# Kernel tuning notes

Hardware: AMD Instinct MI355X
Metric: run time of the kernel (lower is better)

The kernel has to match this reference:

```python
import jax, jax.numpy as jnp
import numpy as np

# static module hyperparameters (match init_kwargs)
DIMS = 1024
HEAD = 16
HD = DIMS // HEAD          # 64
MAX_ITER = 3
MIN_SIZE = 64
MAX_SIZE = 2048
UP_WIN, DOWN_WIN = 1.1, 0.9
UP_DIFF, DOWN_DIFF = 0.05, 0.001
B, T = 2, 1024


def _ln(x, w, eps=1e-5):
    # torch LayerNorm with bias=False (weight only), biased variance
    m = jnp.mean(x, axis=-1, keepdims=True)
    v = jnp.var(x, axis=-1, keepdims=True)
    return (x - m) * jax.lax.rsqrt(v + eps) * w


def setup_inputs() -> dict:
    key = jax.random.key(0)
    ks = jax.random.split(key, 12)

    def lin_w(k, o, i):
        return (jax.random.normal(k, (o, i), dtype=jnp.float32) / np.sqrt(i)).astype(jnp.float32)

    return {
        "x": jax.random.normal(ks[0], (B, T, DIMS), dtype=jnp.float32),
        "Wq": lin_w(ks[1], DIMS, DIMS), "bq": jnp.zeros((DIMS,), jnp.float32),
        "Wk": lin_w(ks[2], DIMS, DIMS),
        "Wv": lin_w(ks[3], DIMS, DIMS), "bv": jnp.zeros((DIMS,), jnp.float32),
        "Wo": lin_w(ks[4], DIMS, DIMS), "bo": jnp.zeros((DIMS,), jnp.float32),
        "lna_w": jnp.ones((DIMS,), jnp.float32),
        "lnb_w": jnp.ones((DIMS,), jnp.float32),
        "lnc_w": jnp.ones((HD,), jnp.float32),
        "lnd_w": jnp.ones((HD,), jnp.float32),
        "lq_w": lin_w(ks[5], HD, HD), "lq_b": jnp.zeros((HD,), jnp.float32),
        "lk_w": lin_w(ks[6], HD, HD), "lk_b": jnp.zeros((HD,), jnp.float32),
        "lv_w": lin_w(ks[7], HD, HD), "lv_b": jnp.zeros((HD,), jnp.float32),
        "threshold": jnp.float32(0.01),
        "temp_base": jnp.float32(1.0),
        "factor": jnp.float32(0.1),
    }


def _focus(x, Wq, bq, Wk, Wv, bv, Wo, bo, lna_w, lnb_w, lnc_w, lnd_w,
           lq_w, lq_b, lk_w, lk_b, lv_w, lv_b, threshold, temp_base, factor):
    b, t, d = x.shape
    q = _ln(x, lna_w) @ Wq.T + bq
    kk = _ln(x, lnb_w) @ Wk.T
    v = _ln(x, lnb_w) @ Wv.T + bv
    sc = HD ** (-0.25)

    def _shape(u):
        return u.reshape(b, t, HEAD, HD).transpose(0, 2, 1, 3)  # [B,H,T,hd]

    q_full = _shape(q * sc)
    k_full = _shape(kk * sc)
    v_full = _shape(v)

    # .item() calls in torch detach these from the graph
    thr = jax.lax.stop_gradient(threshold)
    fac = jax.lax.stop_gradient(factor)
    t0 = jax.lax.stop_gradient(temp_base)

    cw0 = jnp.int32(max(min(t, MAX_SIZE), MIN_SIZE))
    inv_sqrt_e = jnp.float32(1.0 / np.sqrt(HD))  # SDPA default scale
    pos = jnp.arange(t)

    def step(carry, i):
        qcur, prev, attn, cw, temp, done = carry
        # LocalOut projections over full length (out-of-window part masked below)
        qp = qcur @ lq_w.T + lq_b
        kp = k_full @ lk_w.T + lk_b
        vp = v_full @ lv_w.T + lv_b
        sq = _ln(qp, lnc_w)
        sk = _ln(kp, lnd_w)
        tscale = jnp.where(temp > 0, jax.lax.rsqrt(temp), jnp.float32(1.0))
        sq = sq * tscale
        scores = jnp.einsum('bhqd,bhkd->bhqk', sq, sk) * inv_sqrt_e
        in_win = pos < cw
        scores = jnp.where(in_win[None, None, None, :], scores, -jnp.inf)
        probs = jax.nn.softmax(scores, axis=-1)
        out = jnp.einsum('bhqk,bhkd->bhqd', probs, vp)
        # rows >= cur_win stay zero (iter_out buffer semantics)
        iter_out = jnp.where(in_win[None, None, :, None], out, 0.0)

        diff = jnp.mean(jnp.abs(iter_out - prev))
        converged = (diff < thr + fac * diff) & (i > 0)
        upd = (~done) & (~converged)            # continue iterating
        new_done = done | converged

        attn_n = jnp.where(done, attn, iter_out)
        prev_n = jnp.where(upd, iter_out, prev)
        qcur_n = jnp.where(upd, qcur + iter_out, qcur)
        # _next_win
        up = (cw.astype(jnp.float32) * UP_WIN).astype(jnp.int32)
        down = (cw.astype(jnp.float32) * DOWN_WIN).astype(jnp.int32)
        nw = jnp.where(diff > UP_DIFF, up,
                       jnp.where((diff < DOWN_DIFF) & (cw > MIN_SIZE), down, cw))
        nw = jnp.clip(nw, MIN_SIZE, t)
        cw_n = jnp.where(upd, nw, cw)
        temp_n = jnp.where(upd, temp + jnp.float32(0.005), temp)
        return (qcur_n, prev_n, attn_n, cw_n, temp_n, new_done), None

    zeros = jnp.zeros_like(q_full)
    carry0 = (q_full, zeros, zeros, cw0, t0, jnp.array(False))
    (_, _, attn_out, _, _, _), _ = jax.lax.scan(step, carry0, jnp.arange(MAX_ITER))

    output = attn_out.transpose(0, 2, 1, 3).reshape(b, t, d)
    return output @ Wo.T + bo


def reference(x, Wq, bq, Wk, Wv, bv, Wo, bo, lna_w, lnb_w, lnc_w, lnd_w,
              lq_w, lq_b, lk_w, lk_b, lv_w, lv_b, threshold, temp_base, factor):
    return _focus(x, Wq, bq, Wk, Wv, bv, Wo, bo, lna_w, lnb_w, lnc_w, lnd_w,
                  lq_w, lq_b, lk_w, lk_b, lv_w, lv_b, threshold, temp_base, factor)
```

## Files before the change

kernel.cpp:

```cpp
#include <hip/hip_runtime.h>
#include <hip/hip_bf16.h>

#define BDIM 2
#define TDIM 1024
#define DDIM 1024
#define HDIM 16
#define HD   64
#define RROWS (BDIM * TDIM)
#define BH    (BDIM * HDIM)
#define NHE   (BH * TDIM * HD)
#define NHE4  (NHE / 4)
#define DIFF_BLOCKS 512
#define L2E 1.4426950408889634f

typedef __attribute__((ext_vector_type(8))) short short8v;
typedef __attribute__((ext_vector_type(4))) short short4v;
typedef __attribute__((ext_vector_type(8))) _Float16 half8v;
typedef __attribute__((ext_vector_type(4))) _Float16 half4v;
typedef __attribute__((ext_vector_type(4))) float f32x4;

struct FState {
  int   cw;
  float temp;
  int   done;
  int   upd;
  int   done_prev;
  float thr;
  float fac;
  int   pad;
};

static __device__ __forceinline__ unsigned short f2bf(float x) {
  __hip_bfloat16 h = __float2bfloat16(x);
  return __builtin_bit_cast(unsigned short, h);
}
static __device__ __forceinline__ void gload16(const void* g, void* l) {
  __builtin_amdgcn_global_load_lds(
      (const __attribute__((address_space(1))) void*)g,
      (__attribute__((address_space(3))) void*)l, 16, 0, 0);
}

__global__ void init_kernel(FState* st, const float* thr, const float* tb, const float* fac) {
  if (threadIdx.x == 0 && blockIdx.x == 0) {
    st->cw = TDIM;
    st->temp = tb[0];
    st->done = 0;
    st->done_prev = 0;
    st->upd = 1;
    st->thr = thr[0];
    st->fac = fac[0];
  }
}

__global__ __launch_bounds__(256) void ln_x_kernel(
    const float* __restrict__ x, const float* __restrict__ wa, const float* __restrict__ wb,
    _Float16* __restrict__ xaH, _Float16* __restrict__ xbH)
{
  const int row = blockIdx.x;
  const int tid = threadIdx.x;
  const float4 v = reinterpret_cast<const float4*>(x + (size_t)row * DDIM)[tid];
  float s = v.x + v.y + v.z + v.w;
  float q = v.x * v.x + v.y * v.y + v.z * v.z + v.w * v.w;
#pragma unroll
  for (int off = 1; off < 64; off <<= 1) {
    s += __shfl_xor(s, off);
    q += __shfl_xor(q, off);
  }
  __shared__ float ss[4], qq[4];
  const int lane = tid & 63, wv = tid >> 6;
  if (lane == 0) { ss[wv] = s; qq[wv] = q; }
  __syncthreads();
  s = ss[0] + ss[1] + ss[2] + ss[3];
  q = qq[0] + qq[1] + qq[2] + qq[3];
  const float mean = s * (1.0f / DDIM);
  const float var  = q * (1.0f / DDIM) - mean * mean;
  const float inv  = rsqrtf(var + 1e-5f);
  const float4 a4 = reinterpret_cast<const float4*>(wa)[tid];
  const float4 b4 = reinterpret_cast<const float4*>(wb)[tid];
  const float hv[4] = { (v.x - mean) * inv, (v.y - mean) * inv,
                        (v.z - mean) * inv, (v.w - mean) * inv };
  const float av[4] = { a4.x, a4.y, a4.z, a4.w };
  const float bv[4] = { b4.x, b4.y, b4.z, b4.w };
  half4v ha, hb;
#pragma unroll
  for (int j = 0; j < 4; ++j) {
    ha[j] = (_Float16)(hv[j] * av[j]);
    hb[j] = (_Float16)(hv[j] * bv[j]);
  }
  *reinterpret_cast<half4v*>(xaH + (size_t)row * DDIM + tid * 4) = ha;
  *reinterpret_cast<half4v*>(xbH + (size_t)row * DDIM + tid * 4) = hb;
}

__global__ __launch_bounds__(256) void w_cvt_kernel(
    const float* __restrict__ W0, const float* __restrict__ W1,
    const float* __restrict__ W2, const float* __restrict__ W3,
    const float* __restrict__ W4,
    _Float16* __restrict__ O0, _Float16* __restrict__ O1,
    _Float16* __restrict__ O2, _Float16* __restrict__ O3,
    _Float16* __restrict__ O4)
{
  const float* W; _Float16* O;
  switch (blockIdx.y) {
    case 0:  W = W0; O = O0; break;
    case 1:  W = W1; O = O1; break;
    case 2:  W = W2; O = O2; break;
    case 3:  W = W3; O = O3; break;
    default:
      if (blockIdx.x >= 4) return;
      W = W4; O = O4; break;
  }
  const int r = blockIdx.x;
  const int tid = threadIdx.x;
  const float4 v = reinterpret_cast<const float4*>(W + (size_t)r * 1024)[tid];
  half4v h;
  h[0] = (_Float16)v.x; h[1] = (_Float16)v.y;
  h[2] = (_Float16)v.z; h[3] = (_Float16)v.w;
  *reinterpret_cast<half4v*>(O + (size_t)r * 1024 + tid * 4) = h;
}

template<int CMODE>
__global__ __launch_bounds__(256) void gemm_mfma_kernel(
    const _Float16* __restrict__ A0, const _Float16* __restrict__ W0,
    const float* __restrict__ b0, float* __restrict__ C0, float s0,
    const _Float16* __restrict__ A1, const _Float16* __restrict__ W1,
    const float* __restrict__ b1, float* __restrict__ C1, float s1,
    const _Float16* __restrict__ A2, const _Float16* __restrict__ W2,
    const float* __restrict__ b2, float* __restrict__ C2, float s2)
{
  const _Float16* A; const _Float16* W; const float* bias; float* C; float scale;
  switch (blockIdx.z) {
    case 0:  A = A0; W = W0; bias = b0; C = C0; scale = s0; break;
    case 1:  A = A1; W = W1; bias = b1; C = C1; scale = s1; break;
    default: A = A2; W = W2; bias = b2; C = C2; scale = s2; break;
  }
  __shared__ __align__(16) _Float16 As[128 * 32];
  __shared__ __align__(16) _Float16 Ws[128 * 32];
  const int tid = threadIdx.x;
  const int wv = tid >> 6, lane = tid & 63;
  const int wm = wv >> 1, wn = wv & 1;
  const int bm = blockIdx.x;
  const int bn = blockIdx.y;

  const _Float16* gA[2]; const _Float16* gW[2];
  _Float16* lA[2]; _Float16* lW[2];
#pragma unroll
  for (int j = 0; j < 2; ++j) {
    const int chunk = wv * 2 + j;
    const int r = chunk * 16 + (lane >> 2);
    const int ce = (lane & 3) * 8;
    gA[j] = A + (size_t)(bm * 128 + r) * 1024 + ce;
    gW[j] = W + (size_t)(bn * 128 + r) * 1024 + ce;
    lA[j] = As + chunk * 512;
    lW[j] = Ws + chunk * 512;
  }

  f32x4 acc[4][4] = {};
  const int rb = lane & 15;
  const int kb = (lane >> 4) * 8;

  for (int ks = 0; ks < 1024; ks += 32) {
    __syncthreads();
#pragma unroll
    for (int j = 0; j < 2; ++j) {
      gload16(gA[j] + ks, lA[j]);
      gload16(gW[j] + ks, lW[j]);
    }
    __syncthreads();
    half8v af[4], wf[4];
#pragma unroll
    for (int f = 0; f < 4; ++f) {
      af[f] = *reinterpret_cast<const half8v*>(As + (wm * 64 + f * 16 + rb) * 32 + kb);
      wf[f] = *reinterpret_cast<const half8v*>(Ws + (wn * 64 + f * 16 + rb) * 32 + kb);
    }
#pragma unroll
    for (int i = 0; i < 4; ++i)
#pragma unroll
      for (int j2 = 0; j2 < 4; ++j2)
        acc[i][j2] = __builtin_amdgcn_mfma_f32_16x16x32_f16(af[i], wf[j2], acc[i][j2], 0, 0, 0);
  }

#pragma unroll
  for (int j2 = 0; j2 < 4; ++j2) {
    const int n = bn * 128 + wn * 64 + j2 * 16 + (lane & 15);
    const float bv_ = bias ? bias[n] : 0.0f;
#pragma unroll
    for (int i = 0; i < 4; ++i) {
#pragma unroll
      for (int r = 0; r < 4; ++r) {
        const int m = bm * 128 + wm * 64 + i * 16 + (lane >> 4) * 4 + r;
        const float v = (acc[i][j2][r] + bv_) * scale;
        size_t ci;
        if constexpr (CMODE == 0) {
          ci = (size_t)m * 1024 + n;
        } else {
          const int b = m >> 10, t = m & (TDIM - 1);
          ci = ((size_t)(b * HDIM + (n >> 6)) * TDIM + t) * HD + (n & 63);
        }
        C[ci] = v;
      }
    }
  }
}

template<int OUT_MODE, bool DO_LN>
static __device__ __forceinline__ void headproj_body(
    const float* __restrict__ in, unsigned short* __restrict__ out,
    const float* __restrict__ w, const float* __restrict__ bias,
    const float* __restrict__ lnw, float* wl, unsigned short* tT)
{
  const int tid = threadIdx.x;
  for (int idx = tid; idx < 4096; idx += 256) {
    const int d = idx >> 6, i = idx & 63;
    wl[i * 65 + d] = w[idx];
  }
  const int lane = tid & 63, wv = tid >> 6;
  const float bd = bias[lane];
  float lw = 1.0f;
  if constexpr (DO_LN) lw = lnw[lane];
  __syncthreads();
  const int rowBase = blockIdx.x * 32 + wv * 8;
  for (int rr = 0; rr < 8; ++rr) {
    const int row = rowBase + rr;
    const float h = in[(size_t)row * HD + lane];
    float y = bd;
#pragma unroll
    for (int i = 0; i < 64; ++i) {
      const float hv = __uint_as_float((unsigned)__builtin_amdgcn_readlane((int)__float_as_uint(h), i));
      y += wl[i * 65 + lane] * hv;
    }
    if constexpr (DO_LN) {
      float s = y;
#pragma unroll
      for (int off = 1; off < 64; off <<= 1) s += __shfl_xor(s, off);
      const float mean = s * (1.0f / 64.0f);
      const float t0 = y - mean;
      float v2 = t0 * t0;
#pragma unroll
      for (int off = 1; off < 64; off <<= 1) v2 += __shfl_xor(v2, off);
      y = t0 * rsqrtf(v2 * (1.0f / 64.0f) + 1e-5f) * lw;
    }
    if constexpr (OUT_MODE == 0) {
      out[(size_t)row * HD + lane] = f2bf(y);
    } else {
      tT[lane * 34 + wv * 8 + rr] = f2bf(y);
    }
  }
  if constexpr (OUT_MODE == 1) {
    __syncthreads();
    const int hd = tid >> 2, tseg = (tid & 3) * 8;
    const int r0 = blockIdx.x * 32;
    const int bh = r0 >> 10, t0 = r0 & (TDIM - 1);
    short8v v;
#pragma unroll
    for (int i = 0; i < 8; ++i) v[i] = (short)tT[hd * 34 + tseg + i];
    *reinterpret_cast<short8v*>(out + ((size_t)bh * HD + hd) * TDIM + t0 + tseg) = v;
  }
}

__global__ __launch_bounds__(256) void headproj_kv_kernel(
    const float* __restrict__ kin, unsigned short* __restrict__ skb,
    const float* __restrict__ lkw, const float* __restrict__ lkb,
    const float* __restrict__ lnd,
    const float* __restrict__ vin, unsigned short* __restrict__ vpT,
    const float* __restrict__ lvw, const float* __restrict__ lvb)
{
  __shared__ float wl[64 * 65];
  __shared__ unsigned short tT[64 * 34];
  if (blockIdx.y == 0)
    headproj_body<0, true >(kin, skb, lkw, lkb, lnd, wl, tT);
  else
    headproj_body<1, false>(vin, vpT, lvw, lvb, (const float*)nullptr, wl, tT);
}

__global__ __launch_bounds__(512) void attn_mfma_kernel(
    const float* __restrict__ qcur, const unsigned short* __restrict__ sk,
    const unsigned short* __restrict__ vpT, float* __restrict__ io,
    const float* __restrict__ prev, _Float16* __restrict__ attnH,
    const _Float16* __restrict__ lqwH, const float* __restrict__ lqb,
    const float* __restrict__ lnc, float* __restrict__ partials,
    const FState* __restrict__ st, int is_first)
{
  if (st->done) return;
  const int lid = blockIdx.x;
  const int xcd = lid & 7;
  const int rr_ = lid >> 3;
  const int qb  = rr_ & 15;
  const int bh  = (rr_ >> 4) * 8 + xcd;

  const int cw = st->cw;
  const int tid = threadIdx.x;
  const int wv = tid >> 6, lane = tid & 63;
  const int wq = wv & 3, wk = wv >> 2;
  const int ql = lane & 15, hi = lane >> 4;
  const int qbase = qb * 64 + wq * 16;
  const int q = qbase + ql;
  const size_t baseRow = (size_t)bh * TDIM * HD;
  const size_t baseT   = (size_t)bh * HD * TDIM;
  float* orow = io + baseRow + (size_t)q * HD;
  const float* prow = prev + baseRow + (size_t)q * HD;
  float* qcrow = const_cast<float*>(qcur) + baseRow + (size_t)q * HD;
  const bool wvalid = (qbase < cw);
  _Float16* arow = attnH + (size_t)((bh >> 4) * TDIM + q) * 1024 + (bh & 15) * HD;

  __shared__ __align__(16) unsigned char KV[2][2][2][8192];
  __shared__ __align__(16) unsigned char PJ[8][2048];
  float* wred = reinterpret_cast<float*>(&KV[1][1][0][0]);

  const int sub  = lane >> 3;
  const int colB = (lane & 7) * 16;
  const int scol = (colB ^ (sub << 4)) >> 1;

  const int kb0 = wk * 512;
  const unsigned short* kSrc0 = sk  + baseRow + (size_t)(kb0 + wq * 16 + sub) * HD + scol;
  const unsigned short* vSrc0 = vpT + baseT  + (size_t)(wq * 16 + sub) * TDIM + scol;

  unsigned char* pj = (unsigned char*)PJ[wv];
  const unsigned swz8 = (unsigned)((ql & 7) << 4);

  const int nch0 = (min(cw, 512) + 63) >> 6;
  const int nch1 = (cw > 512) ? ((cw - 512 + 63) >> 6) : 0;
  const int nchOwn = wk ? nch1 : nch0;

  if (nchOwn > 0) {
#pragma unroll
    for (int jj = 0; jj < 2; ++jj) {
      gload16(kSrc0 + (size_t)(jj * 8) * HD, &KV[wk][0][0][(wq * 2 + jj) * 1024]);
      gload16(vSrc0 + (size_t)(jj * 8) * TDIM + kb0, &KV[wk][0][1][(wq * 2 + jj) * 1024]);
    }
  }

  short8v qf0, qf1;
  if (wvalid) {
    const float tp = st->temp;
    const float ts = (tp > 0.0f ? rsqrtf(tp) : 1.0f) * 0.125f;
    half8v qh0, qh1;
    {
      const f32x4 a0 = *reinterpret_cast<const f32x4*>(qcrow + hi * 8);
      const f32x4 a1 = *reinterpret_cast<const f32x4*>(qcrow + hi * 8 + 4);
      const f32x4 b0 = *reinterpret_cast<const f32x4*>(qcrow + 32 + hi * 8);
      const f32x4 b1 = *reinterpret_cast<const f32x4*>(qcrow + 32 + hi * 8 + 4);
#pragma unroll
      for (int j = 0; j < 4; ++j) {
        qh0[j] = (_Float16)a0[j]; qh0[4 + j] = (_Float16)a1[j];
        qh1[j] = (_Float16)b0[j]; qh1[4 + j] = (_Float16)b1[j];
      }
    }
    f32x4 sp[4];
#pragma unroll
    for (int f = 0; f < 4; ++f) {
      const half8v a0 = *reinterpret_cast<const half8v*>(lqwH + (f * 16 + ql) * 64 + hi * 8);
      const half8v a1 = *reinterpret_cast<const half8v*>(lqwH + (f * 16 + ql) * 64 + 32 + hi * 8);
      f32x4 acc = {};
      acc = __builtin_amdgcn_mfma_f32_16x16x32_f16(a0, qh0, acc, 0, 0, 0);
      acc = __builtin_amdgcn_mfma_f32_16x16x32_f16(a1, qh1, acc, 0, 0, 0);
      sp[f] = acc;
    }
    float sum = 0.f;
#pragma unroll
    for (int f = 0; f < 4; ++f) {
      const f32x4 b4 = *reinterpret_cast<const f32x4*>(lqb + f * 16 + hi * 4);
      sp[f] += b4;
      sum += (sp[f][0] + sp[f][1]) + (sp[f][2] + sp[f][3]);
    }
    sum += __shfl_xor(sum, 16);
    sum += __shfl_xor(sum, 32);
    const float mean = sum * (1.0f / 64.0f);
    float vs = 0.f;
#pragma unroll
    for (int f = 0; f < 4; ++f) {
#pragma unroll
      for (int r = 0; r < 4; ++r) {
        const float t0 = sp[f][r] - mean;
        sp[f][r] = t0;
        vs += t0 * t0;
      }
    }
    vs += __shfl_xor(vs, 16);
    vs += __shfl_xor(vs, 32);
    const float inv = rsqrtf(vs * (1.0f / 64.0f) + 1e-5f);
    const unsigned wb = (unsigned)(ql * 128 + hi * 8);
#pragma unroll
    for (int f = 0; f < 4; ++f) {
      const f32x4 lc = *reinterpret_cast<const f32x4*>(lnc + f * 16 + hi * 4);
      const float y0 = sp[f][0] * inv * lc[0] * ts;
      const float y1 = sp[f][1] * inv * lc[1] * ts;
      const float y2 = sp[f][2] * inv * lc[2] * ts;
      const float y3 = sp[f][3] * inv * lc[3] * ts;
      *reinterpret_cast<unsigned*>(pj + ((wb + f * 32)     ^ swz8)) =
          (unsigned)f2bf(y0) | ((unsigned)f2bf(y1) << 16);
      *reinterpret_cast<unsigned*>(pj + ((wb + f * 32 + 4) ^ swz8)) =
          (unsigned)f2bf(y2) | ((unsigned)f2bf(y3) << 16);
    }
    qf0 = *reinterpret_cast<short8v*>(pj + ((unsigned)(ql * 128 + hi * 16) ^ swz8));
    qf1 = *reinterpret_cast<short8v*>(pj + ((unsigned)(ql * 128 + 64 + hi * 16) ^ swz8));
  }
  __syncthreads();

  float m = -1e30f, l = 0.f;
  f32x4 o[4] = {};
  int cur = 0;
  for (int ch = 0; ch < nch0; ++ch) {
    if (ch + 1 < nchOwn) {
      const size_t kn = (size_t)(ch + 1) * 64;
#pragma unroll
      for (int jj = 0; jj < 2; ++jj) {
        gload16(kSrc0 + (kn + (size_t)(jj * 8)) * HD, &KV[wk][cur ^ 1][0][(wq * 2 + jj) * 1024]);
        gload16(vSrc0 + (size_t)(jj * 8) * TDIM + kb0 + kn, &KV[wk][cur ^ 1][1][(wq * 2 + jj) * 1024]);
      }
    }
    if (wvalid && ch < nchOwn) {
      const int k0 = kb0 + ch * 64;
      const unsigned char* kt = &KV[wk][cur][0][0];
      const unsigned char* vt = &KV[wk][cur][1][0];
      f32x4 s[4];
#pragma unroll
      for (int f = 0; f < 4; ++f) {
        const unsigned rb = (unsigned)((f * 16 + ql) * 128);
        const short8v a0 = *reinterpret_cast<const short8v*>(kt + rb + ((unsigned)(hi * 16) ^ swz8));
        const short8v a1 = *reinterpret_cast<const short8v*>(kt + rb + ((unsigned)(64 + hi * 16) ^ swz8));
        f32x4 acc = {};
        acc = __builtin_amdgcn_mfma_f32_16x16x32_bf16(a0, qf0, acc, 0, 0, 0);
        acc = __builtin_amdgcn_mfma_f32_16x16x32_bf16(a1, qf1, acc, 0, 0, 0);
        s[f] = acc;
      }
      float mc = -1e30f;
      if (k0 + 64 > cw) {
#pragma unroll
        for (int f = 0; f < 4; ++f)
#pragma unroll
          for (int r = 0; r < 4; ++r) {
            float v = s[f][r];
            if (k0 + f * 16 + hi * 4 + r >= cw) v = -1e30f;
            s[f][r] = v;
            mc = fmaxf(mc, v);
          }
      } else {
#pragma unroll
        for (int f = 0; f < 4; ++f)
#pragma unroll
          for (int r = 0; r < 4; ++r) mc = fmaxf(mc, s[f][r]);
      }
      mc = fmaxf(mc, __shfl_xor(mc, 16));
      mc = fmaxf(mc, __shfl_xor(mc, 32));
      if (__any(mc > m + 8.0f)) {
        const float mn = fmaxf(m, mc);
        const float c = __builtin_amdgcn_exp2f((m - mn) * L2E);
        l *= c;
#pragma unroll
        for (int f = 0; f < 4; ++f) o[f] *= c;
        m = mn;
      }
      float ls = 0.f;
      unsigned pk[8];
#pragma unroll
      for (int f = 0; f < 4; ++f) {
        const float p0 = __builtin_amdgcn_exp2f((s[f][0] - m) * L2E);
        const float p1 = __builtin_amdgcn_exp2f((s[f][1] - m) * L2E);
        const float p2 = __builtin_amdgcn_exp2f((s[f][2] - m) * L2E);
        const float p3 = __builtin_amdgcn_exp2f((s[f][3] - m) * L2E);
        ls += (p0 + p1) + (p2 + p3);
        pk[f * 2]     = (unsigned)f2bf(p0) | ((unsigned)f2bf(p1) << 16);
        pk[f * 2 + 1] = (unsigned)f2bf(p2) | ((unsigned)f2bf(p3) << 16);
      }
      ls += __shfl_xor(ls, 16);
      ls += __shfl_xor(ls, 32);
      l += ls;
      const unsigned wb = (unsigned)(ql * 128 + hi * 8);
#pragma unroll
      for (int f = 0; f < 4; ++f) {
        *reinterpret_cast<unsigned*>(pj + ((wb + f * 32)     ^ swz8)) = pk[f * 2];
        *reinterpret_cast<unsigned*>(pj + ((wb + f * 32 + 4) ^ swz8)) = pk[f * 2 + 1];
      }
#pragma unroll
      for (int kh = 0; kh < 2; ++kh) {
        const short8v pb = *reinterpret_cast<short8v*>(
            pj + ((unsigned)(ql * 128 + kh * 64 + hi * 16) ^ swz8));
#pragma unroll
        for (int f = 0; f < 4; ++f) {
          const unsigned rb = (unsigned)((f * 16 + ql) * 128);
          const short8v av = *reinterpret_cast<const short8v*>(
              vt + rb + ((unsigned)(kh * 64 + hi * 16) ^ swz8));
          o[f] = __builtin_amdgcn_mfma_f32_16x16x32_bf16(av, pb, o[f], 0, 0, 0);
        }
      }
    }
    __syncthreads();
    cur ^= 1;
  }

  float* Obuf = reinterpret_cast<float*>(&KV[0][0][0][0]);
  if (wk == 1 && wvalid) {
    if (hi == 0) {
      Obuf[4352 + wq * 16 + ql] = m;
      Obuf[4416 + wq * 16 + ql] = l;
    }
#pragma unroll
    for (int f = 0; f < 4; ++f)
      *reinterpret_cast<f32x4*>(&Obuf[(wq * 16 + ql) * 68 + f * 16 + hi * 4]) = o[f];
  }
  __syncthreads();

  float pd = 0.0f;
  if (wk == 0) {
    if (wvalid) {
      const float m1 = Obuf[4352 + wq * 16 + ql];
      const float l1 = Obuf[4416 + wq * 16 + ql];
      const float mn = fmaxf(m, m1);
      const float c0 = __builtin_amdgcn_exp2f((m - mn) * L2E);
      const float c1 = __builtin_amdgcn_exp2f((m1 - mn) * L2E);
      const float lt = l * c0 + l1 * c1;
      const bool valid = (q < cw);
      const float invl = valid ? (1.0f / lt) : 0.0f;
#pragma unroll
      for (int f = 0; f < 4; ++f) {
        const f32x4 o1 = *reinterpret_cast<const f32x4*>(&Obuf[(wq * 16 + ql) * 68 + f * 16 + hi * 4]);
        const f32x4 vo = (o[f] * c0 + o1 * c1) * invl;
        *reinterpret_cast<f32x4*>(orow + f * 16 + hi * 4) = vo;
        half4v h4;
        h4[0] = (_Float16)vo[0]; h4[1] = (_Float16)vo[1];
        h4[2] = (_Float16)vo[2]; h4[3] = (_Float16)vo[3];
        *reinterpret_cast<half4v*>(arow + f * 16 + hi * 4) = h4;
        const f32x4 qv = *reinterpret_cast<const f32x4*>(qcrow + f * 16 + hi * 4);
        *reinterpret_cast<f32x4*>(qcrow + f * 16 + hi * 4) = qv + vo;
        if (!is_first) {
          const f32x4 pv = *reinterpret_cast<const f32x4*>(prow + f * 16 + hi * 4);
          pd += fabsf(vo[0] - pv[0]) + fabsf(vo[1] - pv[1]) +
                fabsf(vo[2] - pv[2]) + fabsf(vo[3] - pv[3]);
        } else {
          pd += fabsf(vo[0]) + fabsf(vo[1]) + fabsf(vo[2]) + fabsf(vo[3]);
        }
      }
    } else {
      const f32x4 z = {0.f, 0.f, 0.f, 0.f};
      const half4v hz = { (_Float16)0.f, (_Float16)0.f, (_Float16)0.f, (_Float16)0.f };
#pragma unroll
      for (int f = 0; f < 4; ++f) {
        *reinterpret_cast<f32x4*>(orow + f * 16 + hi * 4) = z;
        *reinterpret_cast<half4v*>(arow + f * 16 + hi * 4) = hz;
        if (!is_first) {
          const f32x4 pv = *reinterpret_cast<const f32x4*>(prow + f * 16 + hi * 4);
          pd += fabsf(pv[0]) + fabsf(pv[1]) + fabsf(pv[2]) + fabsf(pv[3]);
        }
      }
    }
  }

#pragma unroll
  for (int off = 1; off < 64; off <<= 1) pd += __shfl_xor(pd, off);
  if (lane == 0) wred[wv] = pd;
  __syncthreads();
  if (tid == 0)
    partials[lid] = wred[0] + wred[1] + wred[2] + wred[3] +
                    wred[4] + wred[5] + wred[6] + wred[7];
}

__global__ __launch_bounds__(256) void state_update_kernel(
    FState* __restrict__ st, const float* __restrict__ partials, int iter)
{
  const int tid = threadIdx.x;
  float s = 0.0f;
  for (int i = tid; i < DIFF_BLOCKS; i += 256) s += partials[i];
  __shared__ float red[256];
  red[tid] = s;
  __syncthreads();
  for (int off = 128; off > 0; off >>= 1) {
    if (tid < off) red[tid] += red[tid + off];
    __syncthreads();
  }
  if (tid == 0) {
    const int done_prev = st->done;
    st->done_prev = done_prev;
    if (!done_prev) {
      const float diff = red[0] * (1.0f / (float)NHE);
      const bool conv = (diff < st->thr + st->fac * diff) && (iter > 0);
      st->upd  = conv ? 0 : 1;
      st->done = conv ? 1 : 0;
      if (!conv) {
        const int cw = st->cw;
        const int up = (int)((float)cw * 1.1f);
        const int dn = (int)((float)cw * 0.9f);
        int nw = (diff > 0.05f) ? up : ((diff < 0.001f && cw > 64) ? dn : cw);
        nw = nw < 64 ? 64 : (nw > TDIM ? TDIM : nw);
        st->cw = nw;
        st->temp += 0.005f;
      }
    } else {
      st->upd = 0;
    }
  }
}

extern "C" void kernel_launch(void* const* d_in, const int* in_sizes, int n_in,
                              void* d_out, int out_size, void* d_ws, size_t ws_size,
                              hipStream_t stream)
{
  const float* x   = (const float*)d_in[0];
  const float* Wq  = (const float*)d_in[1];
  const float* bq  = (const float*)d_in[2];
  const float* Wk  = (const float*)d_in[3];
  const float* Wv  = (const float*)d_in[4];
  const float* bv  = (const float*)d_in[5];
  const float* Wo  = (const float*)d_in[6];
  const float* bo  = (const float*)d_in[7];
  const float* lna = (const float*)d_in[8];
  const float* lnb = (const float*)d_in[9];
  const float* lnc = (const float*)d_in[10];
  const float* lnd = (const float*)d_in[11];
  const float* lqw = (const float*)d_in[12];
  const float* lqb = (const float*)d_in[13];
  const float* lkw = (const float*)d_in[14];
  const float* lkb = (const float*)d_in[15];
  const float* lvw = (const float*)d_in[16];
  const float* lvb = (const float*)d_in[17];
  const float* thr = (const float*)d_in[18];
  const float* tb  = (const float*)d_in[19];
  const float* fac = (const float*)d_in[20];
  float* out = (float*)d_out;

  float* f0   = (float*)d_ws;
  float* qcur = f0;
  float* io0  = f0 + (size_t)NHE;
  float* io1  = f0 + 2 * (size_t)NHE;
  _Float16* h0   = (_Float16*)(f0 + 3 * (size_t)NHE);
  _Float16* xaH  = h0;
  _Float16* attnH = h0;
  _Float16* xbH  = h0 + (size_t)RROWS * 1024;
  _Float16* WqH  = xbH + (size_t)RROWS * 1024;
  _Float16* WkH  = WqH + (size_t)1048576;
  _Float16* WvH  = WkH + (size_t)1048576;
  _Float16* WoH  = WvH + (size_t)1048576;
  _Float16* lqwH = WoH + (size_t)1048576;
  unsigned short* skb = (unsigned short*)(lqwH + 4096);
  unsigned short* vpT = skb + (size_t)NHE;
  float* partials = (float*)(vpT + (size_t)NHE);
  FState* st = (FState*)(partials + DIFF_BLOCKS);

  constexpr float SC = 0.35355339059327379f;

  hipLaunchKernelGGL(init_kernel, dim3(1), dim3(64), 0, stream, st, thr, tb, fac);
  hipLaunchKernelGGL(ln_x_kernel, dim3(RROWS), dim3(256), 0, stream, x, lna, lnb, xaH, xbH);
  hipLaunchKernelGGL(w_cvt_kernel, dim3(1024, 5), dim3(256), 0, stream,
                     Wq, Wk, Wv, Wo, lqw, WqH, WkH, WvH, WoH, lqwH);

  hipLaunchKernelGGL((gemm_mfma_kernel<1>), dim3(16, 8, 3), dim3(256), 0, stream,
                     xaH, WqH, bq, qcur, SC,
                     xbH, WkH, (const float*)nullptr, io0, SC,
                     xbH, WvH, bv, io1, 1.0f);

  hipLaunchKernelGGL(headproj_kv_kernel, dim3(1024, 2), dim3(256), 0, stream,
                     io0, skb, lkw, lkb, lnd, io1, vpT, lvw, lvb);

  for (int it = 0; it < 3; ++it) {
    float* io   = (it & 1) ? io1 : io0;
    float* prev = (it & 1) ? io0 : io1;
    hipLaunchKernelGGL(attn_mfma_kernel, dim3(DIFF_BLOCKS), dim3(512), 0, stream,
                       qcur, skb, vpT, io, prev, attnH, lqwH, lqb, lnc,
                       partials, st, it == 0 ? 1 : 0);
    hipLaunchKernelGGL(state_update_kernel, dim3(1), dim3(256), 0, stream,
                       st, partials, it);
  }

  hipLaunchKernelGGL((gemm_mfma_kernel<0>), dim3(16, 8, 1), dim3(256), 0, stream,
                     attnH, WoH, bo, out, 1.0f,
                     attnH, WoH, bo, out, 1.0f,
                     attnH, WoH, bo, out, 1.0f);
}
```

Before: 161.3 us.

## Merge prep kernels, fold state update into attention via atomics, halve GEMM N-tile

```diff
diff --git a/kernel.cpp b/kernel.cpp
--- a/kernel.cpp
+++ b/kernel.cpp
@@ -40,24 +40,59 @@
       (__attribute__((address_space(3))) void*)l, 16, 0, 0);
 }
 
-__global__ void init_kernel(FState* st, const float* thr, const float* tb, const float* fac) {
-  if (threadIdx.x == 0 && blockIdx.x == 0) {
-    st->cw = TDIM;
-    st->temp = tb[0];
-    st->done = 0;
-    st->done_prev = 0;
-    st->upd = 1;
-    st->thr = thr[0];
-    st->fac = fac[0];
-  }
-}
-
-__global__ __launch_bounds__(256) void ln_x_kernel(
+__global__ __launch_bounds__(256) void prep_kernel(
     const float* __restrict__ x, const float* __restrict__ wa, const float* __restrict__ wb,
-    _Float16* __restrict__ xaH, _Float16* __restrict__ xbH)
+    _Float16* __restrict__ xaH, _Float16* __restrict__ xbH,
+    const float* __restrict__ W0, const float* __restrict__ W1,
+    const float* __restrict__ W2, const float* __restrict__ W3,
+    const float* __restrict__ W4,
+    _Float16* __restrict__ O0, _Float16* __restrict__ O1,
+    _Float16* __restrict__ O2, _Float16* __restrict__ O3,
+    _Float16* __restrict__ O4,
+    FState* st, float* accF, unsigned* cnt,
+    const float* thr, const float* tb, const float* fac)
 {
-  const int row = blockIdx.x;
+  const int bid = blockIdx.x;
   const int tid = threadIdx.x;
+
+  if (bid >= 6148) {
+    if (tid == 0) {
+      st->cw = TDIM;
+      st->temp = tb[0];
+      st->done = 0;
+      st->done_prev = 0;
+      st->upd = 1;
+      st->thr = thr[0];
+      st->fac = fac[0];
+      accF[0] = 0.f; accF[1] = 0.f; accF[2] = 0.f;
+      cnt[0] = 0u; cnt[1] = 0u; cnt[2] = 0u;
+    }
+    return;
+  }
+
+  if (bid >= 2048) {
+    const int idx = bid - 2048;
+    const float* W; _Float16* O; int r;
+    if (bid >= 6144) { W = W4; O = O4; r = bid - 6144; }
+    else {
+      const int mat = idx >> 10;
+      r = idx & 1023;
+      switch (mat) {
+        case 0:  W = W0; O = O0; break;
+        case 1:  W = W1; O = O1; break;
+        case 2:  W = W2; O = O2; break;
+        default: W = W3; O = O3; break;
+      }
+    }
+    const float4 v = reinterpret_cast<const float4*>(W + (size_t)r * 1024)[tid];
+    half4v h;
+    h[0] = (_Float16)v.x; h[1] = (_Float16)v.y;
+    h[2] = (_Float16)v.z; h[3] = (_Float16)v.w;
+    *reinterpret_cast<half4v*>(O + (size_t)r * 1024 + tid * 4) = h;
+    return;
+  }
+
+  const int row = bid;
   const float4 v = reinterpret_cast<const float4*>(x + (size_t)row * DDIM)[tid];
   float s = v.x + v.y + v.z + v.w;
   float q = v.x * v.x + v.y * v.y + v.z * v.z + v.w * v.w;
@@ -91,33 +126,6 @@
   *reinterpret_cast<half4v*>(xbH + (size_t)row * DDIM + tid * 4) = hb;
 }
 
-__global__ __launch_bounds__(256) void w_cvt_kernel(
-    const float* __restrict__ W0, const float* __restrict__ W1,
-    const float* __restrict__ W2, const float* __restrict__ W3,
-    const float* __restrict__ W4,
-    _Float16* __restrict__ O0, _Float16* __restrict__ O1,
-    _Float16* __restrict__ O2, _Float16* __restrict__ O3,
-    _Float16* __restrict__ O4)
-{
-  const float* W; _Float16* O;
-  switch (blockIdx.y) {
-    case 0:  W = W0; O = O0; break;
-    case 1:  W = W1; O = O1; break;
-    case 2:  W = W2; O = O2; break;
-    case 3:  W = W3; O = O3; break;
-    default:
-      if (blockIdx.x >= 4) return;
-      W = W4; O = O4; break;
-  }
-  const int r = blockIdx.x;
-  const int tid = threadIdx.x;
-  const float4 v = reinterpret_cast<const float4*>(W + (size_t)r * 1024)[tid];
-  half4v h;
-  h[0] = (_Float16)v.x; h[1] = (_Float16)v.y;
-  h[2] = (_Float16)v.z; h[3] = (_Float16)v.w;
-  *reinterpret_cast<half4v*>(O + (size_t)r * 1024 + tid * 4) = h;
-}
-
 template<int CMODE>
 __global__ __launch_bounds__(256) void gemm_mfma_kernel(
     const _Float16* __restrict__ A0, const _Float16* __restrict__ W0,
@@ -134,54 +142,53 @@
     default: A = A2; W = W2; bias = b2; C = C2; scale = s2; break;
   }
   __shared__ __align__(16) _Float16 As[128 * 32];
-  __shared__ __align__(16) _Float16 Ws[128 * 32];
+  __shared__ __align__(16) _Float16 Ws[64 * 32];
   const int tid = threadIdx.x;
   const int wv = tid >> 6, lane = tid & 63;
   const int wm = wv >> 1, wn = wv & 1;
   const int bm = blockIdx.x;
   const int bn = blockIdx.y;
 
-  const _Float16* gA[2]; const _Float16* gW[2];
-  _Float16* lA[2]; _Float16* lW[2];
+  const _Float16* gA[2];
+  _Float16* lA[2];
 #pragma unroll
   for (int j = 0; j < 2; ++j) {
     const int chunk = wv * 2 + j;
     const int r = chunk * 16 + (lane >> 2);
     const int ce = (lane & 3) * 8;
     gA[j] = A + (size_t)(bm * 128 + r) * 1024 + ce;
-    gW[j] = W + (size_t)(bn * 128 + r) * 1024 + ce;
     lA[j] = As + chunk * 512;
-    lW[j] = Ws + chunk * 512;
-  }
-
-  f32x4 acc[4][4] = {};
+  }
+  const _Float16* gW = W + (size_t)(bn * 64 + wv * 16 + (lane >> 2)) * 1024 + (lane & 3) * 8;
+  _Float16* lW = Ws + wv * 512;
+
+  f32x4 acc[4][2] = {};
   const int rb = lane & 15;
   const int kb = (lane >> 4) * 8;
 
   for (int ks = 0; ks < 1024; ks += 32) {
     __syncthreads();
 #pragma unroll
-    for (int j = 0; j < 2; ++j) {
-      gload16(gA[j] + ks, lA[j]);
-      gload16(gW[j] + ks, lW[j]);
-    }
+    for (int j = 0; j < 2; ++j) gload16(gA[j] + ks, lA[j]);
+    gload16(gW + ks, lW);
     __syncthreads();
-    half8v af[4], wf[4];
-#pragma unroll
-    for (int f = 0; f < 4; ++f) {
+    half8v af[4], wf[2];
+#pragma unroll
+    for (int f = 0; f < 4; ++f)
       af[f] = *reinterpret_cast<const half8v*>(As + (wm * 64 + f * 16 + rb) * 32 + kb);
-      wf[f] = *reinterpret_cast<const half8v*>(Ws + (wn * 64 + f * 16 + rb) * 32 + kb);
-    }
+#pragma unroll
+    for (int f = 0; f < 2; ++f)
+      wf[f] = *reinterpret_cast<const half8v*>(Ws + (wn * 32 + f * 16 + rb) * 32 + kb);
 #pragma unroll
     for (int i = 0; i < 4; ++i)
 #pragma unroll
-      for (int j2 = 0; j2 < 4; ++j2)
+      for (int j2 = 0; j2 < 2; ++j2)
         acc[i][j2] = __builtin_amdgcn_mfma_f32_16x16x32_f16(af[i], wf[j2], acc[i][j2], 0, 0, 0);
   }
 
 #pragma unroll
-  for (int j2 = 0; j2 < 4; ++j2) {
-    const int n = bn * 128 + wn * 64 + j2 * 16 + (lane & 15);
+  for (int j2 = 0; j2 < 2; ++j2) {
+    const int n = bn * 64 + wn * 32 + j2 * 16 + (lane & 15);
     const float bv_ = bias ? bias[n] : 0.0f;
 #pragma unroll
     for (int i = 0; i < 4; ++i) {
@@ -277,10 +284,11 @@
     const unsigned short* __restrict__ vpT, float* __restrict__ io,
     const float* __restrict__ prev, _Float16* __restrict__ attnH,
     const _Float16* __restrict__ lqwH, const float* __restrict__ lqb,
-    const float* __restrict__ lnc, float* __restrict__ partials,
-    const FState* __restrict__ st, int is_first)
+    const float* __restrict__ lnc, float* __restrict__ accF,
+    unsigned* __restrict__ cnt, FState* __restrict__ st, int it)
 {
   if (st->done) return;
+  const int is_first = (it == 0);
   const int lid = blockIdx.x;
   const int xcd = lid & 7;
   const int rr_ = lid >> 3;
@@ -549,43 +557,29 @@
   for (int off = 1; off < 64; off <<= 1) pd += __shfl_xor(pd, off);
   if (lane == 0) wred[wv] = pd;
   __syncthreads();
-  if (tid == 0)
-    partials[lid] = wred[0] + wred[1] + wred[2] + wred[3] +
-                    wred[4] + wred[5] + wred[6] + wred[7];
-}
-
-__global__ __launch_bounds__(256) void state_update_kernel(
-    FState* __restrict__ st, const float* __restrict__ partials, int iter)
-{
-  const int tid = threadIdx.x;
-  float s = 0.0f;
-  for (int i = tid; i < DIFF_BLOCKS; i += 256) s += partials[i];
-  __shared__ float red[256];
-  red[tid] = s;
-  __syncthreads();
-  for (int off = 128; off > 0; off >>= 1) {
-    if (tid < off) red[tid] += red[tid + off];
-    __syncthreads();
-  }
+
   if (tid == 0) {
-    const int done_prev = st->done;
-    st->done_prev = done_prev;
-    if (!done_prev) {
-      const float diff = red[0] * (1.0f / (float)NHE);
-      const bool conv = (diff < st->thr + st->fac * diff) && (iter > 0);
-      st->upd  = conv ? 0 : 1;
+    const float blockSum = wred[0] + wred[1] + wred[2] + wred[3] +
+                           wred[4] + wred[5] + wred[6] + wred[7];
+    __hip_atomic_fetch_add(&accF[it], blockSum, __ATOMIC_RELAXED,
+                           __HIP_MEMORY_SCOPE_AGENT);
+    const unsigned old = __hip_atomic_fetch_add(&cnt[it], 1u, __ATOMIC_ACQ_REL,
+                                                __HIP_MEMORY_SCOPE_AGENT);
+    if (old == DIFF_BLOCKS - 1) {
+      const float total = __hip_atomic_load(&accF[it], __ATOMIC_ACQUIRE,
+                                            __HIP_MEMORY_SCOPE_AGENT);
+      const float diff = total * (1.0f / (float)NHE);
+      const bool conv = (diff < st->thr + st->fac * diff) && (it > 0);
       st->done = conv ? 1 : 0;
       if (!conv) {
-        const int cw = st->cw;
-        const int up = (int)((float)cw * 1.1f);
-        const int dn = (int)((float)cw * 0.9f);
-        int nw = (diff > 0.05f) ? up : ((diff < 0.001f && cw > 64) ? dn : cw);
+        const int cwv = st->cw;
+        const int up = (int)((float)cwv * 1.1f);
+        const int dn = (int)((float)cwv * 0.9f);
+        int nw = (diff > 0.05f) ? up : ((diff < 0.001f && cwv > 64) ? dn : cwv);
         nw = nw < 64 ? 64 : (nw > TDIM ? TDIM : nw);
         st->cw = nw;
         st->temp += 0.005f;
       }
-    } else {
-      st->upd = 0;
     }
   }
 }
@@ -632,17 +626,18 @@
   _Float16* lqwH = WoH + (size_t)1048576;
   unsigned short* skb = (unsigned short*)(lqwH + 4096);
   unsigned short* vpT = skb + (size_t)NHE;
-  float* partials = (float*)(vpT + (size_t)NHE);
-  FState* st = (FState*)(partials + DIFF_BLOCKS);
+  float* accF = (float*)(vpT + (size_t)NHE);
+  unsigned* cnt = (unsigned*)(accF + 4);
+  FState* st = (FState*)(cnt + 4);
 
   constexpr float SC = 0.35355339059327379f;
 
-  hipLaunchKernelGGL(init_kernel, dim3(1), dim3(64), 0, stream, st, thr, tb, fac);
-  hipLaunchKernelGGL(ln_x_kernel, dim3(RROWS), dim3(256), 0, stream, x, lna, lnb, xaH, xbH);
-  hipLaunchKernelGGL(w_cvt_kernel, dim3(1024, 5), dim3(256), 0, stream,
-                     Wq, Wk, Wv, Wo, lqw, WqH, WkH, WvH, WoH, lqwH);
-
-  hipLaunchKernelGGL((gemm_mfma_kernel<1>), dim3(16, 8, 3), dim3(256), 0, stream,
+  hipLaunchKernelGGL(prep_kernel, dim3(6149), dim3(256), 0, stream,
+                     x, lna, lnb, xaH, xbH,
+                     Wq, Wk, Wv, Wo, lqw, WqH, WkH, WvH, WoH, lqwH,
+                     st, accF, cnt, thr, tb, fac);
+
+  hipLaunchKernelGGL((gemm_mfma_kernel<1>), dim3(16, 16, 3), dim3(256), 0, stream,
                      xaH, WqH, bq, qcur, SC,
                      xbH, WkH, (const float*)nullptr, io0, SC,
                      xbH, WvH, bv, io1, 1.0f);
@@ -655,12 +650,10 @@
     float* prev = (it & 1) ? io0 : io1;
     hipLaunchKernelGGL(attn_mfma_kernel, dim3(DIFF_BLOCKS), dim3(512), 0, stream,
                        qcur, skb, vpT, io, prev, attnH, lqwH, lqb, lnc,
-                       partials, st, it == 0 ? 1 : 0);
-    hipLaunchKernelGGL(state_update_kernel, dim3(1), dim3(256), 0, stream,
-                       st, partials, it);
-  }
-
-  hipLaunchKernelGGL((gemm_mfma_kernel<0>), dim3(16, 8, 1), dim3(256), 0, stream,
+                       accF, cnt, st, it);
+  }
+
+  hipLaunchKernelGGL((gemm_mfma_kernel<0>), dim3(16, 16, 1), dim3(256), 0, stream,
                      attnH, WoH, bo, out, 1.0f,
                      attnH, WoH, bo, out, 1.0f,
                      attnH, WoH, bo, out, 1.0f);
```

After: 166.6 us. +3.3%, slower.
